# Optimization experiments

Hardware: AMD Instinct MI355X
Metric: run time of the kernel (lower is better)

The kernel has to match this reference:

```python
import jax, jax.numpy as jnp
import numpy as np

B, N_NODES, N_MEM, DEG, D, R = 64, 50000, 65536, 4, 128, 500
E = N_MEM * DEG


def _mlp2(x, W1, b1, W2, b2):
    # F layer with n_layers=2: Dense(leaky_relu) -> Dense(tanh); tf.nn.leaky_relu alpha=0.2
    h = jax.nn.leaky_relu(x @ W1 + b1, negative_slope=0.2)
    return jnp.tanh(h @ W2 + b2)


def setup_inputs() -> dict:
    key = jax.random.key(0)
    ks = jax.random.split(key, 17)
    eg_e = jax.random.randint(ks[0], (E,), 0, B)
    rel = jax.random.randint(ks[1], (E,), 0, R)
    e2vi = jax.random.randint(ks[2], (E,), 0, N_MEM)
    idx_vi = jax.random.randint(ks[3], (E,), 0, N_MEM)
    # every memorized node receives DEG edges; new_idx_e2vj == idx_vj (DPMPN invariant)
    idx_vj = jnp.tile(jnp.arange(N_MEM), DEG)
    z = jnp.zeros((E,), jnp.int32)
    seen_edges = jnp.stack([eg_e, z, z, rel, idx_vi, idx_vj, e2vi, idx_vj], axis=1).astype(jnp.int32)
    eg_m = jax.random.randint(ks[4], (N_MEM,), 0, B)
    v_m = jax.random.randint(ks[5], (N_MEM,), 0, N_NODES)
    memorized_nodes = jnp.stack([eg_m, v_m], axis=1).astype(jnp.int32)
    s = 0.05
    return {
        'hidden': jax.random.normal(ks[6], (N_MEM, D), jnp.float32),
        'seen_edges': seen_edges,
        'memorized_nodes': memorized_nodes,
        'node_attention': jax.random.uniform(ks[7], (B, N_NODES), jnp.float32),
        'hidden_uncon': jax.random.normal(ks[8], (1, N_NODES, D), jnp.float32),
        'query_head_emb': jax.random.normal(ks[9], (B, D), jnp.float32),
        'query_rel_emb': jax.random.normal(ks[10], (B, D), jnp.float32),
        'rel_table': jax.random.normal(ks[11], (R, D), jnp.float32),
        'msg_W1': jax.random.normal(ks[12], (5 * D, D), jnp.float32) * s,
        'msg_b1': jnp.zeros((D,), jnp.float32),
        'msg_W2': jax.random.normal(ks[13], (D, D), jnp.float32) * s,
        'msg_b2': jnp.zeros((D,), jnp.float32),
        'hid_W1': jax.random.normal(ks[14], (5 * D, D), jnp.float32) * s,
        'hid_b1': jnp.zeros((D,), jnp.float32),
        'hid_W2': jax.random.normal(ks[15], (D, D), jnp.float32) * s,
        'hid_b2': jnp.zeros((D,), jnp.float32),
        'int_W': jax.random.normal(ks[16], (D, D), jnp.float32) * s,
    }


def reference(hidden, seen_edges, memorized_nodes, node_attention, hidden_uncon,
              query_head_emb, query_rel_emb, rel_table,
              msg_W1, msg_b1, msg_W2, msg_b2,
              hid_W1, hid_b1, hid_W2, hid_b2, int_W):
    n_mem = hidden.shape[0]
    # node2edge: gather endpoint features to edges
    eg_e = seen_edges[:, 0]
    hidden_vi = hidden[seen_edges[:, 6]]
    hidden_vj = hidden[seen_edges[:, 7]]
    rel_emb = rel_table[seen_edges[:, 3]]
    qh_e = query_head_emb[eg_e]
    qr_e = query_rel_emb[eg_e]
    msg_in = jnp.concatenate([hidden_vi, rel_emb, hidden_vj, qh_e, qr_e], axis=-1)  # [E, 5D]
    message = _mlp2(msg_in, msg_W1, msg_b1, msg_W2, msg_b2)  # [E, D]
    # aggregate at vj, aggr_op 'mean_v3': unsorted_segment_mean * sqrt(count), then scatter
    idx_vj = seen_edges[:, 5]
    seg_sum = jax.ops.segment_sum(message, idx_vj, num_segments=n_mem)
    cnt = jax.ops.segment_sum(jnp.ones((E,), message.dtype), idx_vj, num_segments=n_mem)
    aggr = seg_sum * (jnp.sqrt(cnt) / jnp.maximum(cnt, 1.0))[:, None]
    red = jax.ops.segment_max(seen_edges[:, 7], idx_vj, num_segments=n_mem)
    nonempty = cnt > 0
    red = jnp.where(nonempty, red, 0)
    message_aggr = jnp.zeros_like(hidden).at[red].add(jnp.where(nonempty[:, None], aggr, 0.0))
    # unconscious-flow intervention per memorized node
    eg_m = memorized_nodes[:, 0]
    v_m = memorized_nodes[:, 1]
    hu = hidden_uncon[0][v_m]  # [n_mem, D]
    na = node_attention[eg_m, v_m]  # [n_mem]
    hu = (na[:, None] * hu) @ int_W
    qh_m = query_head_emb[eg_m]
    qr_m = query_rel_emb[eg_m]
    upd_in = jnp.concatenate([message_aggr, hidden, hu, qh_m, qr_m], axis=-1)  # [n_mem, 5D]
    update = _mlp2(upd_in, hid_W1, hid_b1, hid_W2, hid_b2)
    return hidden + update
```

## Files before the change

kernel.cpp:

```cpp
#include <hip/hip_runtime.h>
#include <hip/hip_bf16.h>

typedef unsigned short u16;
typedef __attribute__((ext_vector_type(8))) short bf16x8;
typedef __attribute__((ext_vector_type(4))) float f32x4;

#define N_MEM_C 65536
#define NNODES_C 50000
#define DDIM 128
#define BM 128
#define NTHR 1024
#define TIL(t) ((t) * 16384)

__device__ __align__(16) u16 g_WT[7 * 16384];
__device__ __align__(16) float g_relW[500 * 128];
__device__ __align__(16) float g_qsumM[64 * 128];
__device__ __align__(16) float g_qsumH[64 * 128];
__device__ __align__(16) u16 g_hb[(size_t)N_MEM_C * DDIM];
__device__ __align__(16) u16 g_ub[(size_t)NNODES_C * DDIM];

#define SBAR() do { asm volatile("" ::: "memory"); __builtin_amdgcn_s_barrier(); \
                    asm volatile("" ::: "memory"); } while (0)
#define WAIT_VM0() asm volatile("s_waitcnt vmcnt(0)" ::: "memory")
#define WAIT_VM2() asm volatile("s_waitcnt vmcnt(2)" ::: "memory")
#define WAIT_LG0() asm volatile("s_waitcnt lgkmcnt(0)" ::: "memory")

__device__ __forceinline__ u16 f2bf_s(float f) {
  __hip_bfloat16 h = __float2bfloat16(f);
  u16 u; __builtin_memcpy(&u, &h, 2);
  return u;
}
__device__ __forceinline__ unsigned pk2(float a, float b) {
  __hip_bfloat162 h = __float22bfloat162_rn(make_float2(a, b));
  unsigned u; __builtin_memcpy(&u, &h, 4);
  return u;
}
__device__ __forceinline__ float bf2f(u16 u) {
  unsigned v = ((unsigned)u) << 16;
  float f; __builtin_memcpy(&f, &v, 4);
  return f;
}
__device__ __forceinline__ float fast_tanh(float x) {
  float e = __expf(2.0f * x);
  return 1.0f - 2.0f / (e + 1.0f);
}
__device__ __forceinline__ int swz_off(int r, int c) {
  return r * 128 + ((((c >> 3) ^ (r & 7)) << 3) | (c & 7));
}

extern "C" __global__ void prep_all(const float* __restrict__ hidden,
                                    const float* __restrict__ uncon,
                                    const float* __restrict__ msg_W1,
                                    const float* __restrict__ msg_W2,
                                    const float* __restrict__ hid_W1,
                                    const float* __restrict__ hid_W2,
                                    const float* __restrict__ int_W,
                                    const float* __restrict__ rel_table,
                                    const float* __restrict__ qh,
                                    const float* __restrict__ qr) {
  int bid = blockIdx.x;
  if (bid < 7221) {
    const size_t NH = (size_t)N_MEM_C * DDIM / 8;
    size_t i = (size_t)bid * 256 + threadIdx.x;
    const float* src; u16* dst; size_t o;
    if (i < NH) { src = hidden; dst = g_hb; o = i; }
    else { src = uncon; dst = g_ub; o = i - NH; }
    const float4* p = (const float4*)(src + o * 8);
    float4 a = p[0], b = p[1];
    *(uint4*)(dst + o * 8) =
        make_uint4(pk2(a.x, a.y), pk2(a.z, a.w), pk2(b.x, b.y), pk2(b.z, b.w));
  } else if (bid < 7605) {
    int i = (bid - 7221) * 256 + threadIdx.x;
    int t = i >> 14, idx = i & 16383;
    int n = idx >> 7, k = idx & 127;
    const float* src; int dst;
    switch (t) {
      case 0:  src = msg_W1;             dst = TIL(0); break;
      case 1:  src = msg_W1 + 256 * 128; dst = TIL(1); break;
      case 2:  src = msg_W2;             dst = TIL(2); break;
      case 3:  src = hid_W1;             dst = TIL(3); break;
      case 4:  src = hid_W1 + 128 * 128; dst = TIL(4); break;
      default: src = hid_W2;             dst = TIL(6); break;
    }
    g_WT[dst + swz_off(n, k)] = f2bf_s(src[k * 128 + n]);
  } else if (bid < 7669) {
    int i = (bid - 7605) * 256 + threadIdx.x;
    int n = i & 127, q = i >> 7;
    float s = 0.f;
    for (int p = 0; p < 128; ++p)
      s += int_W[q * 128 + p] * hid_W1[(256 + p) * 128 + n];
    g_WT[TIL(5) + swz_off(n, q)] = f2bf_s(s);
  } else if (bid < 7919) {
    int i = (bid - 7669) * 256 + threadIdx.x;
    int r = i >> 7, n = i & 127;
    float s = 0.f;
    for (int k = 0; k < 128; ++k)
      s += rel_table[r * 128 + k] * msg_W1[(128 + k) * 128 + n];
    g_relW[i] = s;
  } else {
    int i = (bid - 7919) * 256 + threadIdx.x;
    int g = i >> 7, n = i & 127;
    float sM = 0.f, sH = 0.f;
    for (int k = 0; k < 128; ++k) {
      float h = qh[g * 128 + k], r = qr[g * 128 + k];
      sM += h * msg_W1[(384 + k) * 128 + n] + r * msg_W1[(512 + k) * 128 + n];
      sH += h * hid_W1[(384 + k) * 128 + n] + r * hid_W1[(512 + k) * 128 + n];
    }
    g_qsumM[i] = sM;
    g_qsumH[i] = sH;
  }
}

__device__ __forceinline__ void gload_rows(u16* lds_tile, const u16* __restrict__ gsrc,
                                           const int* idxArr, int base,
                                           int wid, int lane) {
  int rsub = lane >> 4, s = lane & 15;
#pragma unroll
  for (int k = 0; k < 2; ++k) {
    int r = wid * 8 + k * 4 + rsub;
    int idx = idxArr ? idxArr[r] : (base + r);
    const u16* gp = gsrc + (size_t)idx * DDIM + ((s ^ (r & 7)) << 3);
    u16* lp = lds_tile + (wid * 8 + k * 4) * 128;
    __builtin_amdgcn_global_load_lds((const __attribute__((address_space(1))) void*)gp,
                                     (__attribute__((address_space(3))) void*)lp,
                                     16, 0, 0);
  }
}
__device__ __forceinline__ void gload_lin(u16* lds_tile, const u16* __restrict__ gsrc,
                                          int wid, int lane) {
#pragma unroll
  for (int k = 0; k < 2; ++k) {
    int off = (wid * 2 + k) * 512;
    const u16* gp = gsrc + off + lane * 8;
    u16* lp = lds_tile + off;
    __builtin_amdgcn_global_load_lds((const __attribute__((address_space(1))) void*)gp,
                                     (__attribute__((address_space(3))) void*)lp,
                                     16, 0, 0);
  }
}

__device__ __forceinline__ void gemmS(const u16* A, const u16* W,
                                      f32x4 (&acc)[2][2], int wr, int wc, int l16, int l4) {
  __builtin_amdgcn_s_setprio(1);
#pragma unroll
  for (int ks = 0; ks < 4; ++ks) {
    int gsl = ks * 4 + l4;
    bf16x8 av[2], bv[2];
#pragma unroll
    for (int nr = 0; nr < 2; ++nr) {
      int rW = wc * 32 + nr * 16 + l16;
      bv[nr] = *(const bf16x8*)&W[rW * 128 + ((gsl ^ (rW & 7)) << 3)];
    }
#pragma unroll
    for (int mr = 0; mr < 2; ++mr) {
      int rA = wr * 32 + mr * 16 + l16;
      av[mr] = *(const bf16x8*)&A[rA * 128 + ((gsl ^ (rA & 7)) << 3)];
    }
#pragma unroll
    for (int mr = 0; mr < 2; ++mr)
#pragma unroll
      for (int nr = 0; nr < 2; ++nr)
        acc[mr][nr] = __builtin_amdgcn_mfma_f32_16x16x32_bf16(av[mr], bv[nr], acc[mr][nr], 0, 0, 0);
  }
  __builtin_amdgcn_s_setprio(0);
}

extern "C" __global__ __launch_bounds__(NTHR, 4) void fused_flow(
    const int* __restrict__ seen_edges, const int* __restrict__ memorized,
    const float* __restrict__ node_att,
    const float* __restrict__ msg_b1, const float* __restrict__ msg_b2,
    const float* __restrict__ hid_b1, const float* __restrict__ hid_b2,
    float* __restrict__ out) {
  __shared__ u16 sA0[16384], sA1[16384];
  __shared__ u16 sW0b[16384], sW2b[16384];
  __shared__ int sEg[4][BM], sRel[4][BM], sVi[4][BM];
  __shared__ int sMeg[BM], sMvm[BM];
  __shared__ float sNA[BM];

  const int tid = threadIdx.x;
  const int lane = tid & 63, wid = tid >> 6;
  const int wr = wid >> 2, wc = wid & 3;
  const int l16 = lane & 15, l4 = lane >> 4;
  const int j0 = blockIdx.x * BM;

  float mb1v[2], mb2v[2], hb1v[2], hb2v[2];
#pragma unroll
  for (int nr = 0; nr < 2; ++nr) {
    int col = wc * 32 + nr * 16 + l16;
    mb1v[nr] = msg_b1[col]; mb2v[nr] = msg_b2[col];
    hb1v[nr] = hid_b1[col]; hb2v[nr] = hid_b2[col];
  }

  gload_lin(sW0b, g_WT + TIL(0), wid, lane);
  gload_lin(sW2b, g_WT + TIL(1), wid, lane);
  gload_rows(sA0, g_hb, nullptr, j0, wid, lane);
  if (tid < 512) {
    int t = tid >> 7, r = tid & 127;
    int e = j0 + r + t * N_MEM_C;
    const int4* se = (const int4*)seen_edges + (size_t)e * 2;
    int4 lo = se[0], hi = se[1];
    sEg[t][r] = min(max(lo.x, 0), 63);
    sRel[t][r] = min(max(lo.w, 0), 499);
    sVi[t][r] = min(max(hi.z, 0), N_MEM_C - 1);
  }
  if (tid < BM) {
    int2 mn = ((const int2*)memorized)[j0 + tid];
    int eg = min(max(mn.x, 0), 63);
    int vm = min(max(mn.y, 0), NNODES_C - 1);
    sMeg[tid] = eg; sMvm[tid] = vm;
    sNA[tid] = node_att[(size_t)eg * NNODES_C + vm];
  }
  WAIT_LG0(); SBAR();
  gload_rows(sA1, g_hb, sVi[0], 0, wid, lane);
  WAIT_VM0(); SBAR();

  const f32x4 zero4 = {0.f, 0.f, 0.f, 0.f};
  f32x4 acc_vj[2][2], aggr[2][2];
#pragma unroll
  for (int a = 0; a < 2; ++a)
#pragma unroll
    for (int b = 0; b < 2; ++b) { acc_vj[a][b] = zero4; aggr[a][b] = zero4; }
  gemmS(sA0, sW2b, acc_vj, wr, wc, l16, l4);
  SBAR();
  gload_lin(sW2b, g_WT + TIL(2), wid, lane);
  gload_rows(sA0, g_hb, sVi[1], 0, wid, lane);

#pragma unroll 1
  for (int t = 0; t < 4; ++t) {
    u16* Acur = (t & 1) ? sA0 : sA1;
    f32x4 acc[2][2];
#pragma unroll
    for (int a = 0; a < 2; ++a)
#pragma unroll
      for (int b = 0; b < 2; ++b) acc[a][b] = acc_vj[a][b];
    gemmS(Acur, sW0b, acc, wr, wc, l16, l4);

#pragma unroll
    for (int mr = 0; mr < 2; ++mr)
#pragma unroll
      for (int i = 0; i < 4; ++i) {
        int r = wr * 32 + mr * 16 + l4 * 4 + i;
        const float* pr = g_relW + sRel[t][r] * 128;
        const float* pq = g_qsumM + sEg[t][r] * 128;
#pragma unroll
        for (int nr = 0; nr < 2; ++nr) {
          int c = wc * 32 + nr * 16 + l16;
          acc[mr][nr][i] += pr[c] + pq[c];
        }
      }
    SBAR();

#pragma unroll
    for (int mr = 0; mr < 2; ++mr)
#pragma unroll
      for (int nr = 0; nr < 2; ++nr)
#pragma unroll
        for (int i = 0; i < 4; ++i) {
          float v = acc[mr][nr][i] + mb1v[nr];
          v = (v >= 0.f) ? v : 0.2f * v;
          int r = wr * 32 + mr * 16 + l4 * 4 + i;
          Acur[swz_off(r, wc * 32 + nr * 16 + l16)] = f2bf_s(v);
        }
    WAIT_LG0();
    if (t == 0) { WAIT_VM2(); }
    SBAR();

    f32x4 acc2[2][2];
#pragma unroll
    for (int a = 0; a < 2; ++a)
#pragma unroll
      for (int b = 0; b < 2; ++b) acc2[a][b] = zero4;
    gemmS(Acur, sW2b, acc2, wr, wc, l16, l4);
#pragma unroll
    for (int mr = 0; mr < 2; ++mr)
#pragma unroll
      for (int nr = 0; nr < 2; ++nr)
#pragma unroll
        for (int i = 0; i < 4; ++i)
          aggr[mr][nr][i] += fast_tanh(acc2[mr][nr][i] + mb2v[nr]);
    WAIT_VM0();
    SBAR();
    if (t < 2)
      gload_rows(Acur, g_hb, sVi[t + 2], 0, wid, lane);
  }

  gload_lin(sW0b, g_WT + TIL(3), wid, lane);
  gload_lin(sW2b, g_WT + TIL(4), wid, lane);
  gload_rows(sA0, g_hb, nullptr, j0, wid, lane);
#pragma unroll
  for (int mr = 0; mr < 2; ++mr)
#pragma unroll
    for (int nr = 0; nr < 2; ++nr)
#pragma unroll
      for (int i = 0; i < 4; ++i) {
        int r = wr * 32 + mr * 16 + l4 * 4 + i;
        sA1[swz_off(r, wc * 32 + nr * 16 + l16)] = f2bf_s(0.5f * aggr[mr][nr][i]);
      }
  WAIT_LG0(); WAIT_VM0(); SBAR();

  f32x4 accU[2][2];
#pragma unroll
  for (int a = 0; a < 2; ++a)
#pragma unroll
    for (int b = 0; b < 2; ++b) accU[a][b] = zero4;
  gemmS(sA1, sW0b, accU, wr, wc, l16, l4);
  SBAR();
  gload_lin(sW0b, g_WT + TIL(5), wid, lane);
  gload_rows(sA1, g_ub, sMvm, 0, wid, lane);
  gemmS(sA0, sW2b, accU, wr, wc, l16, l4);
  SBAR();
  gload_lin(sW2b, g_WT + TIL(6), wid, lane);
  WAIT_VM2(); SBAR();

  f32x4 acc2[2][2];
#pragma unroll
  for (int a = 0; a < 2; ++a)
#pragma unroll
    for (int b = 0; b < 2; ++b) acc2[a][b] = zero4;
  gemmS(sA1, sW0b, acc2, wr, wc, l16, l4);
#pragma unroll
  for (int mr = 0; mr < 2; ++mr)
#pragma unroll
    for (int i = 0; i < 4; ++i) {
      int r = wr * 32 + mr * 16 + l4 * 4 + i;
      float na = sNA[r];
      const float* pq = g_qsumH + sMeg[r] * 128;
#pragma unroll
      for (int nr = 0; nr < 2; ++nr)
        accU[mr][nr][i] += na * acc2[mr][nr][i] + pq[wc * 32 + nr * 16 + l16];
    }
#pragma unroll
  for (int mr = 0; mr < 2; ++mr)
#pragma unroll
    for (int nr = 0; nr < 2; ++nr)
#pragma unroll
      for (int i = 0; i < 4; ++i) {
        float v = accU[mr][nr][i] + hb1v[nr];
        v = (v >= 0.f) ? v : 0.2f * v;
        int r = wr * 32 + mr * 16 + l4 * 4 + i;
        sA0[swz_off(r, wc * 32 + nr * 16 + l16)] = f2bf_s(v);
      }
  WAIT_LG0(); WAIT_VM0(); SBAR();

  f32x4 accF[2][2];
#pragma unroll
  for (int a = 0; a < 2; ++a)
#pragma unroll
    for (int b = 0; b < 2; ++b) accF[a][b] = zero4;
  gemmS(sA0, sW2b, accF, wr, wc, l16, l4);

#pragma unroll
  for (int mr = 0; mr < 2; ++mr)
#pragma unroll
    for (int nr = 0; nr < 2; ++nr)
#pragma unroll
      for (int i = 0; i < 4; ++i) {
        int row = j0 + wr * 32 + mr * 16 + l4 * 4 + i;
        int col = wc * 32 + nr * 16 + l16;
        size_t o = (size_t)row * DDIM + col;
        out[o] = bf2f(g_hb[o]) + fast_tanh(accF[mr][nr][i] + hb2v[nr]);
      }
}

extern "C" void kernel_launch(void* const* d_in, const int* in_sizes, int n_in,
                              void* d_out, int out_size, void* d_ws, size_t ws_size,
                              hipStream_t stream) {
  (void)in_sizes; (void)n_in; (void)out_size; (void)d_ws; (void)ws_size;
  const float* hidden       = (const float*)d_in[0];
  const int*   seen_edges   = (const int*)d_in[1];
  const int*   memorized    = (const int*)d_in[2];
  const float* node_att     = (const float*)d_in[3];
  const float* hidden_uncon = (const float*)d_in[4];
  const float* qh           = (const float*)d_in[5];
  const float* qr           = (const float*)d_in[6];
  const float* rel_table    = (const float*)d_in[7];
  const float* msg_W1       = (const float*)d_in[8];
  const float* msg_b1       = (const float*)d_in[9];
  const float* msg_W2       = (const float*)d_in[10];
  const float* msg_b2       = (const float*)d_in[11];
  const float* hid_W1       = (const float*)d_in[12];
  const float* hid_b1       = (const float*)d_in[13];
  const float* hid_W2       = (const float*)d_in[14];
  const float* hid_b2       = (const float*)d_in[15];
  const float* int_W        = (const float*)d_in[16];

  prep_all<<<dim3(7951), dim3(256), 0, stream>>>(
      hidden, hidden_uncon, msg_W1, msg_W2, hid_W1, hid_W2, int_W,
      rel_table, qh, qr);
  fused_flow<<<dim3(N_MEM_C / BM), dim3(NTHR), 0, stream>>>(
      seen_edges, memorized, node_att, msg_b1, msg_b2, hid_b1, hid_b2, (float*)d_out);
}
```

Baseline: 136.7 us.

## Shrink blocks to 64 rows and read GEMM weights directly from global

The fused kernel drops from 128-row, 1024-thread blocks to 64-row, 256-thread blocks, and each wave now computes a 32x64 output tile instead of 32x32. Weight tiles are no longer staged in LDS. They are stored unswizzled in global memory and loaded straight into registers inside the GEMM, so the weight-reload barriers go away and LDS use drops, allowing more blocks per CU. The cost is extra L1/L2 traffic for weights, since every wave rereads them from cache, plus higher register pressure from the larger per-wave accumulator tiles.

```diff
diff --git a/kernel.cpp b/kernel.cpp
--- a/kernel.cpp
+++ b/kernel.cpp
@@ -8,8 +8,9 @@
 #define N_MEM_C 65536
 #define NNODES_C 50000
 #define DDIM 128
-#define BM 128
-#define NTHR 1024
+#define BM 64
+#define NBLK (N_MEM_C / BM)
+#define NTHR 256
 #define TIL(t) ((t) * 16384)
 
 __device__ __align__(16) u16 g_WT[7 * 16384];
@@ -22,7 +23,6 @@
 #define SBAR() do { asm volatile("" ::: "memory"); __builtin_amdgcn_s_barrier(); \
                     asm volatile("" ::: "memory"); } while (0)
 #define WAIT_VM0() asm volatile("s_waitcnt vmcnt(0)" ::: "memory")
-#define WAIT_VM2() asm volatile("s_waitcnt vmcnt(2)" ::: "memory")
 #define WAIT_LG0() asm volatile("s_waitcnt lgkmcnt(0)" ::: "memory")
 
 __device__ __forceinline__ u16 f2bf_s(float f) {
@@ -82,14 +82,14 @@
       case 4:  src = hid_W1 + 128 * 128; dst = TIL(4); break;
       default: src = hid_W2;             dst = TIL(6); break;
     }
-    g_WT[dst + swz_off(n, k)] = f2bf_s(src[k * 128 + n]);
+    g_WT[dst + n * 128 + k] = f2bf_s(src[k * 128 + n]);
   } else if (bid < 7669) {
     int i = (bid - 7605) * 256 + threadIdx.x;
     int n = i & 127, q = i >> 7;
     float s = 0.f;
     for (int p = 0; p < 128; ++p)
       s += int_W[q * 128 + p] * hid_W1[(256 + p) * 128 + n];
-    g_WT[TIL(5) + swz_off(n, q)] = f2bf_s(s);
+    g_WT[TIL(5) + n * 128 + q] = f2bf_s(s);
   } else if (bid < 7919) {
     int i = (bid - 7669) * 256 + threadIdx.x;
     int r = i >> 7, n = i & 127;
@@ -116,41 +116,28 @@
                                            int wid, int lane) {
   int rsub = lane >> 4, s = lane & 15;
 #pragma unroll
-  for (int k = 0; k < 2; ++k) {
-    int r = wid * 8 + k * 4 + rsub;
+  for (int k = 0; k < 4; ++k) {
+    int r = wid * 16 + k * 4 + rsub;
     int idx = idxArr ? idxArr[r] : (base + r);
     const u16* gp = gsrc + (size_t)idx * DDIM + ((s ^ (r & 7)) << 3);
-    u16* lp = lds_tile + (wid * 8 + k * 4) * 128;
+    u16* lp = lds_tile + (wid * 16 + k * 4) * 128;
     __builtin_amdgcn_global_load_lds((const __attribute__((address_space(1))) void*)gp,
                                      (__attribute__((address_space(3))) void*)lp,
                                      16, 0, 0);
   }
 }
-__device__ __forceinline__ void gload_lin(u16* lds_tile, const u16* __restrict__ gsrc,
-                                          int wid, int lane) {
-#pragma unroll
-  for (int k = 0; k < 2; ++k) {
-    int off = (wid * 2 + k) * 512;
-    const u16* gp = gsrc + off + lane * 8;
-    u16* lp = lds_tile + off;
-    __builtin_amdgcn_global_load_lds((const __attribute__((address_space(1))) void*)gp,
-                                     (__attribute__((address_space(3))) void*)lp,
-                                     16, 0, 0);
-  }
-}
-
-__device__ __forceinline__ void gemmS(const u16* A, const u16* W,
-                                      f32x4 (&acc)[2][2], int wr, int wc, int l16, int l4) {
+
+__device__ __forceinline__ void gemmG(const u16* A, const u16* __restrict__ WT,
+                                      f32x4 (&acc)[2][4], int wr, int wc, int l16, int l4) {
+  const u16* wb = WT + (wc * 64 + l16) * 128 + l4 * 8;
   __builtin_amdgcn_s_setprio(1);
 #pragma unroll
   for (int ks = 0; ks < 4; ++ks) {
     int gsl = ks * 4 + l4;
-    bf16x8 av[2], bv[2];
-#pragma unroll
-    for (int nr = 0; nr < 2; ++nr) {
-      int rW = wc * 32 + nr * 16 + l16;
-      bv[nr] = *(const bf16x8*)&W[rW * 128 + ((gsl ^ (rW & 7)) << 3)];
-    }
+    bf16x8 av[2], bv[4];
+#pragma unroll
+    for (int nr = 0; nr < 4; ++nr)
+      bv[nr] = *(const bf16x8*)(wb + nr * 16 * 128 + ks * 32);
 #pragma unroll
     for (int mr = 0; mr < 2; ++mr) {
       int rA = wr * 32 + mr * 16 + l16;
@@ -159,43 +146,40 @@
 #pragma unroll
     for (int mr = 0; mr < 2; ++mr)
 #pragma unroll
-      for (int nr = 0; nr < 2; ++nr)
+      for (int nr = 0; nr < 4; ++nr)
         acc[mr][nr] = __builtin_amdgcn_mfma_f32_16x16x32_bf16(av[mr], bv[nr], acc[mr][nr], 0, 0, 0);
   }
   __builtin_amdgcn_s_setprio(0);
 }
 
-extern "C" __global__ __launch_bounds__(NTHR, 4) void fused_flow(
+extern "C" __global__ __launch_bounds__(NTHR, 3) void fused_flow(
     const int* __restrict__ seen_edges, const int* __restrict__ memorized,
     const float* __restrict__ node_att,
     const float* __restrict__ msg_b1, const float* __restrict__ msg_b2,
     const float* __restrict__ hid_b1, const float* __restrict__ hid_b2,
     float* __restrict__ out) {
-  __shared__ u16 sA0[16384], sA1[16384];
-  __shared__ u16 sW0b[16384], sW2b[16384];
+  __shared__ u16 sA0[BM * 128], sA1[BM * 128];
   __shared__ int sEg[4][BM], sRel[4][BM], sVi[4][BM];
   __shared__ int sMeg[BM], sMvm[BM];
   __shared__ float sNA[BM];
 
   const int tid = threadIdx.x;
   const int lane = tid & 63, wid = tid >> 6;
-  const int wr = wid >> 2, wc = wid & 3;
+  const int wr = wid >> 1, wc = wid & 1;
   const int l16 = lane & 15, l4 = lane >> 4;
   const int j0 = blockIdx.x * BM;
 
-  float mb1v[2], mb2v[2], hb1v[2], hb2v[2];
-#pragma unroll
-  for (int nr = 0; nr < 2; ++nr) {
-    int col = wc * 32 + nr * 16 + l16;
+  float mb1v[4], mb2v[4], hb1v[4], hb2v[4];
+#pragma unroll
+  for (int nr = 0; nr < 4; ++nr) {
+    int col = wc * 64 + nr * 16 + l16;
     mb1v[nr] = msg_b1[col]; mb2v[nr] = msg_b2[col];
     hb1v[nr] = hid_b1[col]; hb2v[nr] = hid_b2[col];
   }
 
-  gload_lin(sW0b, g_WT + TIL(0), wid, lane);
-  gload_lin(sW2b, g_WT + TIL(1), wid, lane);
   gload_rows(sA0, g_hb, nullptr, j0, wid, lane);
-  if (tid < 512) {
-    int t = tid >> 7, r = tid & 127;
+  {
+    int t = tid >> 6, r = tid & 63;
     int e = j0 + r + t * N_MEM_C;
     const int4* se = (const int4*)seen_edges + (size_t)e * 2;
     int4 lo = se[0], hi = se[1];
@@ -215,25 +199,24 @@
   WAIT_VM0(); SBAR();
 
   const f32x4 zero4 = {0.f, 0.f, 0.f, 0.f};
-  f32x4 acc_vj[2][2], aggr[2][2];
+  f32x4 acc_vj[2][4], aggr[2][4];
 #pragma unroll
   for (int a = 0; a < 2; ++a)
 #pragma unroll
-    for (int b = 0; b < 2; ++b) { acc_vj[a][b] = zero4; aggr[a][b] = zero4; }
-  gemmS(sA0, sW2b, acc_vj, wr, wc, l16, l4);
+    for (int b = 0; b < 4; ++b) { acc_vj[a][b] = zero4; aggr[a][b] = zero4; }
+  gemmG(sA0, g_WT + TIL(1), acc_vj, wr, wc, l16, l4);
   SBAR();
-  gload_lin(sW2b, g_WT + TIL(2), wid, lane);
   gload_rows(sA0, g_hb, sVi[1], 0, wid, lane);
 
 #pragma unroll 1
   for (int t = 0; t < 4; ++t) {
     u16* Acur = (t & 1) ? sA0 : sA1;
-    f32x4 acc[2][2];
+    f32x4 acc[2][4];
 #pragma unroll
     for (int a = 0; a < 2; ++a)
 #pragma unroll
-      for (int b = 0; b < 2; ++b) acc[a][b] = acc_vj[a][b];
-    gemmS(Acur, sW0b, acc, wr, wc, l16, l4);
+      for (int b = 0; b < 4; ++b) acc[a][b] = acc_vj[a][b];
+    gemmG(Acur, g_WT + TIL(0), acc, wr, wc, l16, l4);
 
 #pragma unroll
     for (int mr = 0; mr < 2; ++mr)
@@ -243,8 +226,8 @@
         const float* pr = g_relW + sRel[t][r] * 128;
         const float* pq = g_qsumM + sEg[t][r] * 128;
 #pragma unroll
-        for (int nr = 0; nr < 2; ++nr) {
-          int c = wc * 32 + nr * 16 + l16;
+        for (int nr = 0; nr < 4; ++nr) {
+          int c = wc * 64 + nr * 16 + l16;
           acc[mr][nr][i] += pr[c] + pq[c];
         }
       }
@@ -253,28 +236,26 @@
 #pragma unroll
     for (int mr = 0; mr < 2; ++mr)
 #pragma unroll
-      for (int nr = 0; nr < 2; ++nr)
+      for (int nr = 0; nr < 4; ++nr)
 #pragma unroll
         for (int i = 0; i < 4; ++i) {
           float v = acc[mr][nr][i] + mb1v[nr];
           v = (v >= 0.f) ? v : 0.2f * v;
           int r = wr * 32 + mr * 16 + l4 * 4 + i;
-          Acur[swz_off(r, wc * 32 + nr * 16 + l16)] = f2bf_s(v);
+          Acur[swz_off(r, wc * 64 + nr * 16 + l16)] = f2bf_s(v);
         }
-    WAIT_LG0();
-    if (t == 0) { WAIT_VM2(); }
-    SBAR();
-
-    f32x4 acc2[2][2];
+    WAIT_LG0(); SBAR();
+
+    f32x4 acc2[2][4];
 #pragma unroll
     for (int a = 0; a < 2; ++a)
 #pragma unroll
-      for (int b = 0; b < 2; ++b) acc2[a][b] = zero4;
-    gemmS(Acur, sW2b, acc2, wr, wc, l16, l4);
+      for (int b = 0; b < 4; ++b) acc2[a][b] = zero4;
+    gemmG(Acur, g_WT + TIL(2), acc2, wr, wc, l16, l4);
 #pragma unroll
     for (int mr = 0; mr < 2; ++mr)
 #pragma unroll
-      for (int nr = 0; nr < 2; ++nr)
+      for (int nr = 0; nr < 4; ++nr)
 #pragma unroll
         for (int i = 0; i < 4; ++i)
           aggr[mr][nr][i] += fast_tanh(acc2[mr][nr][i] + mb2v[nr]);
@@ -284,40 +265,35 @@
       gload_rows(Acur, g_hb, sVi[t + 2], 0, wid, lane);
   }
 
-  gload_lin(sW0b, g_WT + TIL(3), wid, lane);
-  gload_lin(sW2b, g_WT + TIL(4), wid, lane);
   gload_rows(sA0, g_hb, nullptr, j0, wid, lane);
 #pragma unroll
   for (int mr = 0; mr < 2; ++mr)
 #pragma unroll
-    for (int nr = 0; nr < 2; ++nr)
+    for (int nr = 0; nr < 4; ++nr)
 #pragma unroll
       for (int i = 0; i < 4; ++i) {
         int r = wr * 32 + mr * 16 + l4 * 4 + i;
-        sA1[swz_off(r, wc * 32 + nr * 16 + l16)] = f2bf_s(0.5f * aggr[mr][nr][i]);
+        sA1[swz_off(r, wc * 64 + nr * 16 + l16)] = f2bf_s(0.5f * aggr[mr][nr][i]);
       }
   WAIT_LG0(); WAIT_VM0(); SBAR();
 
-  f32x4 accU[2][2];
+  f32x4 accU[2][4];
 #pragma unroll
   for (int a = 0; a < 2; ++a)
 #pragma unroll
-    for (int b = 0; b < 2; ++b) accU[a][b] = zero4;
-  gemmS(sA1, sW0b, accU, wr, wc, l16, l4);
+    for (int b = 0; b < 4; ++b) accU[a][b] = zero4;
+  gemmG(sA1, g_WT + TIL(3), accU, wr, wc, l16, l4);
+  gemmG(sA0, g_WT + TIL(4), accU, wr, wc, l16, l4);
   SBAR();
-  gload_lin(sW0b, g_WT + TIL(5), wid, lane);
   gload_rows(sA1, g_ub, sMvm, 0, wid, lane);
-  gemmS(sA0, sW2b, accU, wr, wc, l16, l4);
-  SBAR();
-  gload_lin(sW2b, g_WT + TIL(6), wid, lane);
-  WAIT_VM2(); SBAR();
-
-  f32x4 acc2[2][2];
+  WAIT_VM0(); SBAR();
+
+  f32x4 acc2[2][4];
 #pragma unroll
   for (int a = 0; a < 2; ++a)
 #pragma unroll
-    for (int b = 0; b < 2; ++b) acc2[a][b] = zero4;
-  gemmS(sA1, sW0b, acc2, wr, wc, l16, l4);
+    for (int b = 0; b < 4; ++b) acc2[a][b] = zero4;
+  gemmG(sA1, g_WT + TIL(5), acc2, wr, wc, l16, l4);
 #pragma unroll
   for (int mr = 0; mr < 2; ++mr)
 #pragma unroll
@@ -326,37 +302,37 @@
       float na = sNA[r];
       const float* pq = g_qsumH + sMeg[r] * 128;
 #pragma unroll
-      for (int nr = 0; nr < 2; ++nr)
-        accU[mr][nr][i] += na * acc2[mr][nr][i] + pq[wc * 32 + nr * 16 + l16];
+      for (int nr = 0; nr < 4; ++nr)
+        accU[mr][nr][i] += na * acc2[mr][nr][i] + pq[wc * 64 + nr * 16 + l16];
     }
 #pragma unroll
   for (int mr = 0; mr < 2; ++mr)
 #pragma unroll
-    for (int nr = 0; nr < 2; ++nr)
+    for (int nr = 0; nr < 4; ++nr)
 #pragma unroll
       for (int i = 0; i < 4; ++i) {
         float v = accU[mr][nr][i] + hb1v[nr];
         v = (v >= 0.f) ? v : 0.2f * v;
         int r = wr * 32 + mr * 16 + l4 * 4 + i;
-        sA0[swz_off(r, wc * 32 + nr * 16 + l16)] = f2bf_s(v);
+        sA0[swz_off(r, wc * 64 + nr * 16 + l16)] = f2bf_s(v);
       }
-  WAIT_LG0(); WAIT_VM0(); SBAR();
-
-  f32x4 accF[2][2];
+  WAIT_LG0(); SBAR();
+
+  f32x4 accF[2][4];
 #pragma unroll
   for (int a = 0; a < 2; ++a)
 #pragma unroll
-    for (int b = 0; b < 2; ++b) accF[a][b] = zero4;
-  gemmS(sA0, sW2b, accF, wr, wc, l16, l4);
+    for (int b = 0; b < 4; ++b) accF[a][b] = zero4;
+  gemmG(sA0, g_WT + TIL(6), accF, wr, wc, l16, l4);
 
 #pragma unroll
   for (int mr = 0; mr < 2; ++mr)
 #pragma unroll
-    for (int nr = 0; nr < 2; ++nr)
+    for (int nr = 0; nr < 4; ++nr)
 #pragma unroll
       for (int i = 0; i < 4; ++i) {
         int row = j0 + wr * 32 + mr * 16 + l4 * 4 + i;
-        int col = wc * 32 + nr * 16 + l16;
+        int col = wc * 64 + nr * 16 + l16;
         size_t o = (size_t)row * DDIM + col;
         out[o] = bf2f(g_hb[o]) + fast_tanh(accF[mr][nr][i] + hb2v[nr]);
       }
@@ -387,6 +363,6 @@
   prep_all<<<dim3(7951), dim3(256), 0, stream>>>(
       hidden, hidden_uncon, msg_W1, msg_W2, hid_W1, hid_W2, int_W,
       rel_table, qh, qr);
-  fused_flow<<<dim3(N_MEM_C / BM), dim3(NTHR), 0, stream>>>(
+  fused_flow<<<dim3(NBLK), dim3(NTHR), 0, stream>>>(
       seen_edges, memorized, node_att, msg_b1, msg_b2, hid_b1, hid_b2, (float*)d_out);
 }
```

After: 338.4 us. +147.5%, slower.
